# Performance work log

Hardware: AMD Instinct MI355X
Metric: run time of the kernel (lower is better)

The kernel has to match this reference:

```python
import jax, jax.numpy as jnp
import numpy as np

B, N_O, N_Q = 2, 512, 512
POS_DIM, LATENT, HEADS, HEAD_DIM, OUT_DIM = 3, 256, 8, 32, 128
HD = HEADS * HEAD_DIM  # == LATENT here


def _lin(key, fan_in, fan_out):
    return jax.random.normal(key, (fan_in, fan_out), jnp.float32) / np.sqrt(fan_in)


def setup_inputs() -> dict:
    key = jax.random.key(0)
    ks = jax.random.split(key, 12)
    return {
        'h_obs': jax.random.normal(ks[0], (B, N_O, LATENT), jnp.float32),
        'pos_obs': jax.random.uniform(ks[1], (B, N_O, POS_DIM), jnp.float32),
        'pos_query': jax.random.uniform(ks[2], (B, N_Q, POS_DIM), jnp.float32),
        'fw1': _lin(ks[3], LATENT, LATENT), 'fb1': jnp.zeros((LATENT,), jnp.float32),
        'fw2': _lin(ks[4], LATENT, HD), 'fb2': jnp.zeros((HD,), jnp.float32),
        'log_sigma': jnp.zeros((HEADS,), jnp.float32),
        'kw1': _lin(ks[5], POS_DIM * 3, LATENT), 'kb1': jnp.zeros((LATENT,), jnp.float32),
        'kw2': _lin(ks[6], LATENT, HEADS), 'kb2': jnp.zeros((HEADS,), jnp.float32),
        'ow': _lin(ks[7], HD, OUT_DIM), 'ob': jnp.zeros((OUT_DIM,), jnp.float32),
        'vw': _lin(ks[8], HD, OUT_DIM), 'vb': jnp.zeros((OUT_DIM,), jnp.float32),
    }


def reference(h_obs, pos_obs, pos_query, fw1, fb1, fw2, fb2, log_sigma,
              kw1, kb1, kw2, kb2, ow, ob, vw, vb):
    Bv, No, _ = h_obs.shape
    Nq = pos_query.shape[1]
    # feature net -> values [B, H, N_o, D]
    v = jax.nn.relu(h_obs @ fw1 + fb1) @ fw2 + fb2
    v = v.reshape(Bv, No, HEADS, HEAD_DIM).transpose(0, 2, 1, 3)
    # pairwise relative positions [B, Nq, No, P]
    pos_q = pos_query[:, :, None, :]
    pos_o = pos_obs[:, None, :, :]
    rel = pos_q - pos_o
    dist2 = jnp.sum(rel ** 2, axis=-1)  # [B, Nq, No]
    sigma = jnp.exp(log_sigma)[None, :, None, None]
    rbf = jnp.exp(-dist2[:, None] / (sigma ** 2 + 1e-6))  # [B, H, Nq, No]
    # kernel MLP on concatenated pairwise positions [B, Nq, No, 3P] -> [B, H, Nq, No]
    ki = jnp.concatenate([
        jnp.broadcast_to(pos_q, (Bv, Nq, No, POS_DIM)),
        jnp.broadcast_to(pos_o, (Bv, Nq, No, POS_DIM)),
        rel], axis=-1)
    delta = (jax.nn.relu(ki @ kw1 + kb1) @ kw2 + kb2).transpose(0, 3, 1, 2)
    logits = jnp.log(rbf + 1e-8) + delta
    weights = jax.nn.softmax(logits, axis=-1)  # [B, H, Nq, No]
    # weighted mean over observations
    v_mean = jnp.einsum('bhqo,bhod->bhqd', weights, v)  # [B, H, Nq, D]
    h_query = v_mean.transpose(0, 2, 1, 3).reshape(Bv, Nq, HD)
    # weighted variance: sum_o w * (v_o - v_mean)^2
    residual = v[:, :, None, :, :] - v_mean[:, :, :, None, :]  # [B, H, Nq, No, D]
    var = jnp.sum(weights[..., None] * residual ** 2, axis=3)  # [B, H, Nq, D]
    var = var.transpose(0, 2, 1, 3).reshape(Bv, Nq, HD)
    mean = h_query @ ow + ob
    var_out = jax.nn.softplus(var @ vw + vb)
    return (mean, var_out)
```

## Files before the change

### kernel.cpp

```cpp
#include <hip/hip_runtime.h>
#include <math.h>

#define NB 2
#define NO 512
#define NQ 512
#define OUT_DIM 128
#define LPAD 516

typedef __attribute__((ext_vector_type(8))) _Float16 half8;
typedef __attribute__((ext_vector_type(4))) _Float16 half4;
typedef __attribute__((ext_vector_type(4))) float f32x4;

__device__ __forceinline__ float softplus_f(float x) {
  return x > 0.0f ? x + log1pf(expf(-x)) : log1pf(expf(x));
}
__device__ __forceinline__ half8 splat8(_Float16 v) {
  return (half8){v, v, v, v, v, v, v, v};
}
__device__ __forceinline__ half8 fma8(half8 a, half8 b, half8 c) {
  return __builtin_elementwise_fma(a, b, c);
}
__device__ __forceinline__ half8 max8(half8 a, half8 b) {
  return __builtin_elementwise_max(a, b);
}
__device__ __forceinline__ void gll16(const void* g, void* l) {
  __builtin_amdgcn_global_load_lds(
      (const __attribute__((address_space(1))) unsigned int*)g,
      (__attribute__((address_space(3))) unsigned int*)l, 16, 0, 0);
}

__global__ __launch_bounds__(1024) void prep_kernel(
    const float* __restrict__ h_obs, const float* __restrict__ fw1,
    const float* __restrict__ fb1, const float* __restrict__ fw2,
    const float* __restrict__ fb2,
    const float* __restrict__ ow, const float* __restrict__ vw,
    _Float16* __restrict__ VT, _Float16* __restrict__ W2h)
{
  if (blockIdx.x >= 256) {
    const int i  = blockIdx.x - 256;
    const int e0 = (i * 1024 + threadIdx.x) * 2;
    const int k = e0 >> 8, col = e0 & 255;
    float v0 = (col < 128) ? ow[k * 128 + col] : vw[k * 128 + col - 128];
    float v1 = (col + 1 < 128) ? ow[k * 128 + col + 1] : vw[k * 128 + col - 127];
    W2h[e0]     = (_Float16)v0;
    W2h[e0 + 1] = (_Float16)v1;
    return;
  }
  __shared__ float s_red[4][4][256];
  __shared__ float s_hid[4][256];
  const int n  = threadIdx.x & 255;
  const int ks = threadIdx.x >> 8;
  const int r0 = blockIdx.x * 4;
  const int k0 = ks * 64;
  float a0 = 0.f, a1 = 0.f, a2 = 0.f, a3 = 0.f;
  #pragma unroll 8
  for (int kk = 0; kk < 64; ++kk) {
    int k = k0 + kk;
    float w = fw1[k * 256 + n];
    a0 = fmaf(h_obs[(r0 + 0) * 256 + k], w, a0);
    a1 = fmaf(h_obs[(r0 + 1) * 256 + k], w, a1);
    a2 = fmaf(h_obs[(r0 + 2) * 256 + k], w, a2);
    a3 = fmaf(h_obs[(r0 + 3) * 256 + k], w, a3);
  }
  s_red[ks][0][n] = a0; s_red[ks][1][n] = a1;
  s_red[ks][2][n] = a2; s_red[ks][3][n] = a3;
  __syncthreads();
  if (ks == 0) {
    float bb = fb1[n];
    #pragma unroll
    for (int r = 0; r < 4; ++r) {
      float v = s_red[0][r][n] + s_red[1][r][n] + s_red[2][r][n] + s_red[3][r][n] + bb;
      s_hid[r][n] = fmaxf(v, 0.f);
    }
  }
  __syncthreads();
  float c0 = 0.f, c1 = 0.f, c2 = 0.f, c3 = 0.f;
  #pragma unroll 8
  for (int kk = 0; kk < 64; ++kk) {
    int k = k0 + kk;
    float w = fw2[k * 256 + n];
    c0 = fmaf(s_hid[0][k], w, c0);
    c1 = fmaf(s_hid[1][k], w, c1);
    c2 = fmaf(s_hid[2][k], w, c2);
    c3 = fmaf(s_hid[3][k], w, c3);
  }
  __syncthreads();
  s_red[ks][0][n] = c0; s_red[ks][1][n] = c1;
  s_red[ks][2][n] = c2; s_red[ks][3][n] = c3;
  __syncthreads();
  if (ks == 0) {
    float bb = fb2[n];
    float vr[4];
    #pragma unroll
    for (int r = 0; r < 4; ++r)
      vr[r] = s_red[0][r][n] + s_red[1][r][n] + s_red[2][r][n] + s_red[3][r][n] + bb;
    const int h  = n >> 5, d = n & 31;
    const int bb_ = r0 >> 9, o0 = r0 & 511;
    half4 pv;
    #pragma unroll
    for (int r = 0; r < 4; ++r) pv[r] = (_Float16)vr[r];
    *(half4*)(VT + ((size_t)((bb_ * 8 + h) * 32 + d)) * 512 + o0) = pv;
  }
}

__global__ __launch_bounds__(512, 4) void attn_fused(
    const _Float16* __restrict__ VT,
    const _Float16* __restrict__ W2h,
    const float* __restrict__ kw1,
    const float* __restrict__ kb1,
    const float* __restrict__ kw2,
    const float* __restrict__ kb2,
    const float* __restrict__ log_sigma,
    const float* __restrict__ pos_obs,
    const float* __restrict__ pos_query,
    const float* __restrict__ obias, const float* __restrict__ vbias,
    float* __restrict__ out)
{
  __shared__ __align__(16) float s_logits[2][8 * LPAD];
  __shared__ __align__(16) _Float16 s_P16[2][8][520];
  __shared__ half8 s_Bh[512];
  __shared__ __align__(16) float s_pool[256];
  __shared__ __align__(16) float s_po[3][516];
  __shared__ __align__(16) _Float16 s_co[3][264];

  _Float16* s_aq2 = (_Float16*)s_pool;
  float*    s_hvx = (float*)s_po;

  const int t   = threadIdx.x;
  const int bq0 = blockIdx.x * 2;
  const int b   = bq0 >> 9;

  float pqx[2], pqy[2], pqz[2];
  #pragma unroll
  for (int q = 0; q < 2; ++q) {
    pqx[q] = pos_query[(bq0 + q) * 3 + 0];
    pqy[q] = pos_query[(bq0 + q) * 3 + 1];
    pqz[q] = pos_query[(bq0 + q) * 3 + 2];
  }
  {
    const int q = t >> 8, j = t & 255;
    float c0 = kw1[0 * 256 + j] + kw1[6 * 256 + j];
    float c1 = kw1[1 * 256 + j] + kw1[7 * 256 + j];
    float c2 = kw1[2 * 256 + j] + kw1[8 * 256 + j];
    s_aq2[q * 256 + j] = (_Float16)
        fmaf(pqx[q], c0, fmaf(pqy[q], c1, fmaf(pqz[q], c2, kb1[j])));
  }
  if (t < 256) {
    const int j = t;
    s_co[0][j] = (_Float16)(kw1[3 * 256 + j] - kw1[6 * 256 + j]);
    s_co[1][j] = (_Float16)(kw1[4 * 256 + j] - kw1[7 * 256 + j]);
    s_co[2][j] = (_Float16)(kw1[5 * 256 + j] - kw1[8 * 256 + j]);
  }
  {
    const int o = t;
    const float* p = pos_obs + (size_t)(b * NO + o) * 3;
    float px = p[0], py = p[1], pz = p[2];
    s_po[0][o] = px; s_po[1][o] = py; s_po[2][o] = pz;
    float d2q[2];
    #pragma unroll
    for (int q = 0; q < 2; ++q) {
      float r0 = pqx[q] - px, r1 = pqy[q] - py, r2 = pqz[q] - pz;
      d2q[q] = r0 * r0 + r1 * r1 + r2 * r2;
    }
    #pragma unroll
    for (int h = 0; h < 8; ++h) {
      float sg  = __expf(log_sigma[h]);
      float inv = 1.0f / (sg * sg + 1e-6f);
      float kbv = kb2[h];
      s_logits[0][h * LPAD + o] = fmaxf(-d2q[0] * inv, -18.420681f) + kbv;
      s_logits[1][h * LPAD + o] = fmaxf(-d2q[1] * inv, -18.420681f) + kbv;
    }
  }
  {
    const int kstep = t >> 6, lane = t & 63;
    const int nh = lane & 15;
    const int kb_ = kstep * 32 + ((lane >> 4) & 3) * 8;
    half8 b8;
    #pragma unroll
    for (int i = 0; i < 8; ++i) {
      float v = (nh < 8) ? kw2[(kb_ + i) * 8 + nh] : 0.f;
      b8[i] = (_Float16)v;
    }
    s_Bh[kstep * 64 + lane] = b8;
  }
  __syncthreads();

  {
    const int wave = t >> 6, lane = t & 63;
    const int quad = lane >> 4, mrow = lane & 15;
    const int tb   = wave * 4;
    _Float16 pxh[4], pyh[4], pzh[4];
    #pragma unroll
    for (int jt = 0; jt < 4; ++jt) {
      const int o = (tb + jt) * 16 + mrow;
      pxh[jt] = (_Float16)s_po[0][o];
      pyh[jt] = (_Float16)s_po[1][o];
      pzh[jt] = (_Float16)s_po[2][o];
    }
    f32x4 C[2][4];
    #pragma unroll
    for (int q = 0; q < 2; ++q)
      #pragma unroll
      for (int jt = 0; jt < 4; ++jt) C[q][jt] = (f32x4){0.f, 0.f, 0.f, 0.f};

    const half8 z8 = {0, 0, 0, 0, 0, 0, 0, 0};
    #pragma unroll
    for (int kstep = 0; kstep < 8; ++kstep) {
      const int koff = kstep * 32 + quad * 8;
      half8 c0 = *(const half8*)&s_co[0][koff];
      half8 c1 = *(const half8*)&s_co[1][koff];
      half8 c2 = *(const half8*)&s_co[2][koff];
      half8 aq0 = *(const half8*)(s_aq2 + koff);
      half8 aq1 = *(const half8*)(s_aq2 + 256 + koff);
      half8 bh  = s_Bh[kstep * 64 + lane];
      #pragma unroll
      for (int jt = 0; jt < 4; ++jt) {
        half8 ao = fma8(splat8(pxh[jt]), c0,
                   fma8(splat8(pyh[jt]), c1, splat8(pzh[jt]) * c2));
        half8 a0 = max8(aq0 + ao, z8);
        half8 a1 = max8(aq1 + ao, z8);
        C[0][jt] = __builtin_amdgcn_mfma_f32_16x16x32_f16(a0, bh, C[0][jt], 0, 0, 0);
        C[1][jt] = __builtin_amdgcn_mfma_f32_16x16x32_f16(a1, bh, C[1][jt], 0, 0, 0);
      }
    }
    const int hh = lane & 15;
    if (hh < 8) {
      #pragma unroll
      for (int q = 0; q < 2; ++q)
        #pragma unroll
        for (int jt = 0; jt < 4; ++jt) {
          const int ob2 = (tb + jt) * 16 + quad * 4;
          #pragma unroll
          for (int r = 0; r < 4; ++r)
            s_logits[q][hh * LPAD + ob2 + r] += C[q][jt][r];
        }
    }
  }
  __syncthreads();

  {
    const int h = t >> 6, lane = t & 63;
    const int kg = lane >> 4, dl = lane & 15;
    char* stg0 = (char*)s_Bh + h * 1024;
    char* b1   = (char*)&s_logits[0][h * LPAD];
    char* b3   = b1 + 1024;
    char* b2   = (char*)&s_logits[1][h * LPAD];
    const _Float16* vsrc = VT + ((size_t)(b * 8 + h) << 14)
                         + (lane >> 1) * 512 + (lane & 1) * 8;
    gll16(vsrc, stg0);

    float invq0, invq1;
    {
      const float* pl0 = &s_logits[0][h * LPAD];
      const float* pl1 = &s_logits[1][h * LPAD];
      float l0[8], l1[8];
      float m0 = -1e30f, m1 = -1e30f;
      #pragma unroll
      for (int k = 0; k < 8; ++k) {
        l0[k] = pl0[k * 64 + lane];
        l1[k] = pl1[k * 64 + lane];
        m0 = fmaxf(m0, l0[k]);
        m1 = fmaxf(m1, l1[k]);
      }
      #pragma unroll
      for (int off = 32; off >= 1; off >>= 1) {
        m0 = fmaxf(m0, __shfl_xor(m0, off, 64));
        m1 = fmaxf(m1, __shfl_xor(m1, off, 64));
      }
      float s0 = 0.f, s1 = 0.f;
      _Float16* pp0 = &s_P16[0][h][0];
      _Float16* pp1 = &s_P16[1][h][0];
      #pragma unroll
      for (int k = 0; k < 8; ++k) {
        float p0 = __expf(l0[k] - m0);
        float p1 = __expf(l1[k] - m1);
        s0 += p0; s1 += p1;
        pp0[k * 64 + lane] = (_Float16)p0;
        pp1[k * 64 + lane] = (_Float16)p1;
      }
      #pragma unroll
      for (int off = 32; off >= 1; off >>= 1) {
        s0 += __shfl_xor(s0, off, 64);
        s1 += __shfl_xor(s1, off, 64);
      }
      invq0 = 1.0f / s0; invq1 = 1.0f / s1;
    }
    gll16(vsrc + 16, b1);
    gll16(vsrc + 32, b2);
    gll16(vsrc + 48, b3);

    const char* pE = ((kg & 2) ? b1 : stg0) + dl * 32 + (kg & 1) * 16;
    const char* pO = ((kg & 2) ? b3 : b2)   + dl * 32 + (kg & 1) * 16;
    const _Float16* pB = &s_P16[lane & 1][h][0];
    f32x4 Cm0 = {0.f, 0.f, 0.f, 0.f}, Cm1 = Cm0, Cv0 = Cm0, Cv1 = Cm0;
    #pragma unroll
    for (int kp = 0; kp < 8; ++kp) {
      asm volatile("s_waitcnt vmcnt(2)" ::: "memory");
      {
        half8 am0 = *(const half8*)(pE);
        half8 am1 = *(const half8*)(pE + 512);
        half8 pb  = *(const half8*)(pB + (2 * kp) * 32 + kg * 8);
        half8 av0 = am0 * am0;
        half8 av1 = am1 * am1;
        __builtin_amdgcn_s_setprio(1);
        Cm0 = __builtin_amdgcn_mfma_f32_16x16x32_f16(am0, pb, Cm0, 0, 0, 0);
        Cm1 = __builtin_amdgcn_mfma_f32_16x16x32_f16(am1, pb, Cm1, 0, 0, 0);
        Cv0 = __builtin_amdgcn_mfma_f32_16x16x32_f16(av0, pb, Cv0, 0, 0, 0);
        Cv1 = __builtin_amdgcn_mfma_f32_16x16x32_f16(av1, pb, Cv1, 0, 0, 0);
        __builtin_amdgcn_s_setprio(0);
      }
      if (kp < 7) {
        asm volatile("s_waitcnt lgkmcnt(0)" ::: "memory");
        gll16(vsrc + (4 * kp + 4) * 16, stg0);
        gll16(vsrc + (4 * kp + 5) * 16, b1);
      }
      if (kp < 7) asm volatile("s_waitcnt vmcnt(2)" ::: "memory");
      else        asm volatile("s_waitcnt vmcnt(0)" ::: "memory");
      {
        half8 am0 = *(const half8*)(pO);
        half8 am1 = *(const half8*)(pO + 512);
        half8 pb  = *(const half8*)(pB + (2 * kp + 1) * 32 + kg * 8);
        half8 av0 = am0 * am0;
        half8 av1 = am1 * am1;
        __builtin_amdgcn_s_setprio(1);
        Cm0 = __builtin_amdgcn_mfma_f32_16x16x32_f16(am0, pb, Cm0, 0, 0, 0);
        Cm1 = __builtin_amdgcn_mfma_f32_16x16x32_f16(am1, pb, Cm1, 0, 0, 0);
        Cv0 = __builtin_amdgcn_mfma_f32_16x16x32_f16(av0, pb, Cv0, 0, 0, 0);
        Cv1 = __builtin_amdgcn_mfma_f32_16x16x32_f16(av1, pb, Cv1, 0, 0, 0);
        __builtin_amdgcn_s_setprio(0);
      }
      if (kp < 7) {
        asm volatile("s_waitcnt lgkmcnt(0)" ::: "memory");
        gll16(vsrc + (4 * kp + 6) * 16, b2);
        gll16(vsrc + (4 * kp + 7) * 16, b3);
      }
    }
    const int nq = lane & 15;
    if (nq < 2) {
      const float iv = nq ? invq1 : invq0;
      const int dbase = h * 32 + kg * 4;
      f32x4 m0, v0, m1, v1;
      #pragma unroll
      for (int r = 0; r < 4; ++r) {
        float a = Cm0[r] * iv;
        m0[r] = a; v0[r] = fmaxf(Cv0[r] * iv - a * a, 0.f);
        float c = Cm1[r] * iv;
        m1[r] = c; v1[r] = fmaxf(Cv1[r] * iv - c * c, 0.f);
      }
      *(f32x4*)(s_hvx + (nq * 2 + 0) * 256 + dbase)      = m0;
      *(f32x4*)(s_hvx + (nq * 2 + 1) * 256 + dbase)      = v0;
      *(f32x4*)(s_hvx + (nq * 2 + 0) * 256 + dbase + 16) = m1;
      *(f32x4*)(s_hvx + (nq * 2 + 1) * 256 + dbase + 16) = v1;
    }
  }
  __syncthreads();

  {
    const int row = t >> 7, n = t & 127;
    const int m = row & 1, qq = row >> 1;
    const float* X = s_hvx + row * 256;
    const _Float16* Wp = W2h + (m * 128 + n);
    float acc = 0.f;
    #pragma unroll 4
    for (int k0 = 0; k0 < 256; k0 += 8) {
      float4 xa = *(const float4*)&X[k0];
      float4 xb = *(const float4*)&X[k0 + 4];
      acc = fmaf(xa.x, (float)Wp[(k0 + 0) * 256], acc);
      acc = fmaf(xa.y, (float)Wp[(k0 + 1) * 256], acc);
      acc = fmaf(xa.z, (float)Wp[(k0 + 2) * 256], acc);
      acc = fmaf(xa.w, (float)Wp[(k0 + 3) * 256], acc);
      acc = fmaf(xb.x, (float)Wp[(k0 + 4) * 256], acc);
      acc = fmaf(xb.y, (float)Wp[(k0 + 5) * 256], acc);
      acc = fmaf(xb.z, (float)Wp[(k0 + 6) * 256], acc);
      acc = fmaf(xb.w, (float)Wp[(k0 + 7) * 256], acc);
    }
    float v = acc + (m ? vbias[n] : obias[n]);
    if (m) v = softplus_f(v);
    out[(size_t)m * (NB * NQ * OUT_DIM) + (size_t)(bq0 + qq) * OUT_DIM + n] = v;
  }
}

extern "C" void kernel_launch(void* const* d_in, const int* in_sizes, int n_in,
                              void* d_out, int out_size, void* d_ws, size_t ws_size,
                              hipStream_t stream)
{
  const float* h_obs     = (const float*)d_in[0];
  const float* pos_obs   = (const float*)d_in[1];
  const float* pos_query = (const float*)d_in[2];
  const float* fw1       = (const float*)d_in[3];
  const float* fb1       = (const float*)d_in[4];
  const float* fw2       = (const float*)d_in[5];
  const float* fb2       = (const float*)d_in[6];
  const float* log_sigma = (const float*)d_in[7];
  const float* kw1       = (const float*)d_in[8];
  const float* kb1       = (const float*)d_in[9];
  const float* kw2       = (const float*)d_in[10];
  const float* kb2       = (const float*)d_in[11];
  const float* ow        = (const float*)d_in[12];
  const float* ob        = (const float*)d_in[13];
  const float* vw        = (const float*)d_in[14];
  const float* vb        = (const float*)d_in[15];

  float* out = (float*)d_out;
  _Float16* ws = (_Float16*)d_ws;
  _Float16* VT  = ws;
  _Float16* W2h = ws + 262144;

  prep_kernel<<<288, 1024, 0, stream>>>(h_obs, fw1, fb1, fw2, fb2, ow, vw,
                                        VT, W2h);
  attn_fused<<<NB * NQ / 2, 512, 0, stream>>>(VT, W2h, kw1, kb1, kw2, kb2,
                                              log_sigma, pos_obs, pos_query,
                                              ob, vb, out);
}
```

Baseline: 130.4 us.

## Split output projection across waves with LDS-staged async weight loads

The final output projection is restructured. Instead of each thread striding through global W2h with scalar fp16 loads, each wave now owns a 32-row slice of K. It streams its weight rows into reused LDS buffers with async global_load_lds in a 5-deep ring, with the first loads issued before the barrier. Per-wave partial sums are written to LDS and reduced across the 8 waves. The s_P16 layout is transposed to [h][q] so the per-head buffers can be reused as staging space. This adds LDS traffic, a cross-wave reduction and hand-placed waitcnt counting, which is fragile if the counts are wrong.

```diff
diff --git a/kernel.cpp b/kernel.cpp
--- a/kernel.cpp
+++ b/kernel.cpp
@@ -9,6 +9,7 @@
 
 typedef __attribute__((ext_vector_type(8))) _Float16 half8;
 typedef __attribute__((ext_vector_type(4))) _Float16 half4;
+typedef __attribute__((ext_vector_type(2))) _Float16 h2v;
 typedef __attribute__((ext_vector_type(4))) float f32x4;
 
 __device__ __forceinline__ float softplus_f(float x) {
@@ -117,7 +118,7 @@
     float* __restrict__ out)
 {
   __shared__ __align__(16) float s_logits[2][8 * LPAD];
-  __shared__ __align__(16) _Float16 s_P16[2][8][520];
+  __shared__ __align__(16) _Float16 s_P16[8][2][520];
   __shared__ half8 s_Bh[512];
   __shared__ __align__(16) float s_pool[256];
   __shared__ __align__(16) float s_po[3][516];
@@ -268,8 +269,8 @@
         m1 = fmaxf(m1, __shfl_xor(m1, off, 64));
       }
       float s0 = 0.f, s1 = 0.f;
-      _Float16* pp0 = &s_P16[0][h][0];
-      _Float16* pp1 = &s_P16[1][h][0];
+      _Float16* pp0 = &s_P16[h][0][0];
+      _Float16* pp1 = &s_P16[h][1][0];
       #pragma unroll
       for (int k = 0; k < 8; ++k) {
         float p0 = __expf(l0[k] - m0);
@@ -291,7 +292,7 @@
 
     const char* pE = ((kg & 2) ? b1 : stg0) + dl * 32 + (kg & 1) * 16;
     const char* pO = ((kg & 2) ? b3 : b2)   + dl * 32 + (kg & 1) * 16;
-    const _Float16* pB = &s_P16[lane & 1][h][0];
+    const _Float16* pB = &s_P16[h][lane & 1][0];
     f32x4 Cm0 = {0.f, 0.f, 0.f, 0.f}, Cm1 = Cm0, Cv0 = Cm0, Cv1 = Cm0;
     #pragma unroll
     for (int kp = 0; kp < 8; ++kp) {
@@ -352,28 +353,87 @@
       *(f32x4*)(s_hvx + (nq * 2 + 0) * 256 + dbase + 16) = m1;
       *(f32x4*)(s_hvx + (nq * 2 + 1) * 256 + dbase + 16) = v1;
     }
+    asm volatile("s_waitcnt lgkmcnt(0)" ::: "memory");
+    const _Float16* wsrc = W2h + h * 32 * 256 + lane * 8;
+    char* f4B = (char*)&s_P16[h][0][0];
+    gll16(wsrc + 0 * 512, stg0);
+    gll16(wsrc + 1 * 512, f4B);
+    gll16(wsrc + 2 * 512, f4B + 1024);
+    gll16(wsrc + 3 * 512, b1);
+    gll16(wsrc + 4 * 512, b3);
+  }
+  __syncthreads();
+
+  {
+    const int h = t >> 6, l = t & 63;
+    char* f4A = (char*)s_Bh + h * 1024;
+    char* f4B = (char*)&s_P16[h][0][0];
+    char* f4C = f4B + 1024;
+    char* f4D = (char*)&s_logits[0][h * LPAD];
+    char* f4E = f4D + 1024;
+    const _Float16* wsrc = W2h + h * 32 * 256 + l * 8;
+    const float* Xr = s_hvx;
+    float a00 = 0.f, a01 = 0.f, a10 = 0.f, a11 = 0.f;
+    float a20 = 0.f, a21 = 0.f, a30 = 0.f, a31 = 0.f;
+
+#define P4STEP(c, BUF, WN, REFILL)                                          \
+    { asm volatile("s_waitcnt vmcnt(" WN ")" ::: "memory");                 \
+      const char* bp4 = (BUF);                                              \
+      _Pragma("unroll")                                                     \
+      for (int kr = 0; kr < 2; ++kr) {                                      \
+        const int k = h * 32 + (c) * 2 + kr;                                \
+        unsigned uw0 = *(const unsigned*)(bp4 + kr * 512 + l * 4);          \
+        unsigned uw1 = *(const unsigned*)(bp4 + kr * 512 + 256 + l * 4);    \
+        h2v p0 = __builtin_bit_cast(h2v, uw0);                              \
+        h2v p1 = __builtin_bit_cast(h2v, uw1);                              \
+        float w0a = (float)p0.x, w0b = (float)p0.y;                         \
+        float w1a = (float)p1.x, w1b = (float)p1.y;                         \
+        float x0 = Xr[k], x1 = Xr[256 + k];                                 \
+        float x2 = Xr[512 + k], x3 = Xr[768 + k];                           \
+        a00 = fmaf(x0, w0a, a00); a01 = fmaf(x0, w0b, a01);                 \
+        a20 = fmaf(x2, w0a, a20); a21 = fmaf(x2, w0b, a21);                 \
+        a10 = fmaf(x1, w1a, a10); a11 = fmaf(x1, w1b, a11);                 \
+        a30 = fmaf(x3, w1a, a30); a31 = fmaf(x3, w1b, a31);                 \
+      }                                                                     \
+      REFILL }
+#define RFL(c, BUF) \
+      asm volatile("s_waitcnt lgkmcnt(0)" ::: "memory"); \
+      gll16(wsrc + (c) * 512, BUF);
+
+    P4STEP( 0, f4A, "4", RFL( 5, f4A))
+    P4STEP( 1, f4B, "4", RFL( 6, f4B))
+    P4STEP( 2, f4C, "4", RFL( 7, f4C))
+    P4STEP( 3, f4D, "4", RFL( 8, f4D))
+    P4STEP( 4, f4E, "4", RFL( 9, f4E))
+    P4STEP( 5, f4A, "4", RFL(10, f4A))
+    P4STEP( 6, f4B, "4", RFL(11, f4B))
+    P4STEP( 7, f4C, "4", RFL(12, f4C))
+    P4STEP( 8, f4D, "4", RFL(13, f4D))
+    P4STEP( 9, f4E, "4", RFL(14, f4E))
+    P4STEP(10, f4A, "4", RFL(15, f4A))
+    P4STEP(11, f4B, "4", )
+    P4STEP(12, f4C, "3", )
+    P4STEP(13, f4D, "2", )
+    P4STEP(14, f4E, "1", )
+    P4STEP(15, f4A, "0", )
+#undef RFL
+#undef P4STEP
+
+    float* pw = (float*)((char*)s_logits + 8 * LPAD * 4 + h * 2064);
+    pw[0 * 129 + 2 * l] = a00; pw[0 * 129 + 2 * l + 1] = a01;
+    pw[1 * 129 + 2 * l] = a10; pw[1 * 129 + 2 * l + 1] = a11;
+    pw[2 * 129 + 2 * l] = a20; pw[2 * 129 + 2 * l + 1] = a21;
+    pw[3 * 129 + 2 * l] = a30; pw[3 * 129 + 2 * l + 1] = a31;
   }
   __syncthreads();
 
   {
     const int row = t >> 7, n = t & 127;
     const int m = row & 1, qq = row >> 1;
-    const float* X = s_hvx + row * 256;
-    const _Float16* Wp = W2h + (m * 128 + n);
     float acc = 0.f;
-    #pragma unroll 4
-    for (int k0 = 0; k0 < 256; k0 += 8) {
-      float4 xa = *(const float4*)&X[k0];
-      float4 xb = *(const float4*)&X[k0 + 4];
-      acc = fmaf(xa.x, (float)Wp[(k0 + 0) * 256], acc);
-      acc = fmaf(xa.y, (float)Wp[(k0 + 1) * 256], acc);
-      acc = fmaf(xa.z, (float)Wp[(k0 + 2) * 256], acc);
-      acc = fmaf(xa.w, (float)Wp[(k0 + 3) * 256], acc);
-      acc = fmaf(xb.x, (float)Wp[(k0 + 4) * 256], acc);
-      acc = fmaf(xb.y, (float)Wp[(k0 + 5) * 256], acc);
-      acc = fmaf(xb.z, (float)Wp[(k0 + 6) * 256], acc);
-      acc = fmaf(xb.w, (float)Wp[(k0 + 7) * 256], acc);
-    }
+    #pragma unroll
+    for (int w = 0; w < 8; ++w)
+      acc += ((const float*)((char*)s_logits + 8 * LPAD * 4 + w * 2064))[row * 129 + n];
     float v = acc + (m ? vbias[n] : obias[n]);
     if (m) v = softplus_f(v);
     out[(size_t)m * (NB * NQ * OUT_DIM) + (size_t)(bq0 + qq) * OUT_DIM + n] = v;
```

Result: faster. 127.0 us (-2.6%).
